# Performance work log

Hardware: AMD Instinct MI355X
Metric: run time of the kernel (lower is better)

## Reference

```python
import jax, jax.numpy as jnp
import numpy as np

NEG_SLOPE = 0.2   # PyG GATConv default leaky_relu slope
K_TOP = 50        # img_token_len
EPS = 1e-12


def _add_self_loops(ei, n):
    loop = jnp.arange(n, dtype=ei.dtype)
    return jnp.concatenate([ei, jnp.stack([loop, loop])], axis=1)


def _gcn(x, ei, W, b, n):
    ei = _add_self_loops(ei, n)
    src, dst = ei[0], ei[1]
    deg = jax.ops.segment_sum(jnp.ones_like(src, jnp.float32), dst, num_segments=n)
    dinv = jax.lax.rsqrt(jnp.maximum(deg, EPS))
    norm = dinv[src] * dinv[dst]                      # [E+N]
    h = x @ W                                         # [N, H]
    out = jax.ops.segment_sum(h[src] * norm[:, None], dst, num_segments=n)
    return out + b


def _gat(x, ei, W, b, a_src, a_dst, n):
    # PyG GATConv, heads=1, concat=True, with self loops; returns attention
    ei = _add_self_loops(ei, n)
    src, dst = ei[0], ei[1]
    h = x @ W                                         # [N, D]
    asrc = h @ a_src                                  # [N]
    adst = h @ a_dst                                  # [N]
    e = jax.nn.leaky_relu(asrc[src] + adst[dst], NEG_SLOPE)
    # segment softmax over incoming edges of each dst node
    m = jax.ops.segment_max(e, dst, num_segments=n)
    ex = jnp.exp(e - m[dst])
    s = jax.ops.segment_sum(ex, dst, num_segments=n)
    alpha = ex / s[dst]                               # [E+N]
    out = jax.ops.segment_sum(alpha[:, None] * h[src], dst, num_segments=n) + b
    return out, ei, alpha


def _patch_att(ei, alpha, n):
    # fused form of the original per-edge python loop: scatter-add alpha to
    # both endpoints, count contributions, divide (segment mean)
    src, dst = ei[0], ei[1]
    ones = jnp.ones_like(alpha)
    att = jax.ops.segment_sum(alpha, src, num_segments=n) + \
          jax.ops.segment_sum(alpha, dst, num_segments=n)
    cnt = jax.ops.segment_sum(ones, src, num_segments=n) + \
          jax.ops.segment_sum(ones, dst, num_segments=n)
    return att / cnt


def reference(x, edge_index, W_gcn, b_gcn, W_gat, b_gat, a_src, a_dst, W_proj, b_proj):
    B, N, _ = x.shape

    def per_graph(xi, ei):
        h = jax.nn.relu(_gcn(xi, ei, W_gcn, b_gcn, N))        # dropout: eval mode (identity)
        gnn_out, ei_sl, alpha = _gat(h, ei, W_gat, b_gat, a_src, a_dst, N)
        score = _patch_att(ei_sl, alpha, N)
        return gnn_out, score

    emb, scores = jax.vmap(per_graph)(x, edge_index)          # [B,N,256], [B,N]
    emb = emb @ W_proj + b_proj                               # img_proj -> [B,N,1024]
    emb = emb.reshape(-1, emb.shape[-1])                      # [B*N, 1024]
    scores = scores.reshape(-1)                               # [B*N]
    topk_scores, topk_idx = jax.lax.top_k(scores, K_TOP)
    topk_feats = emb[topk_idx]                                # [50, 1024]
    return topk_feats


def setup_inputs() -> dict:
    key = jax.random.key(0)
    ks = jax.random.split(key, 8)
    B, N, E, F, H, D, P = 256, 100, 1600, 2048, 512, 256, 1024
    return {
        "x": jax.random.normal(ks[0], (B, N, F), jnp.float32),
        "edge_index": jax.random.randint(ks[1], (B, 2, E), 0, N, dtype=jnp.int64),
        "W_gcn": jax.random.normal(ks[2], (F, H), jnp.float32) * (1.0 / np.sqrt(F)),
        "b_gcn": jnp.zeros((H,), jnp.float32),
        "W_gat": jax.random.normal(ks[3], (H, D), jnp.float32) * (1.0 / np.sqrt(H)),
        "b_gat": jnp.zeros((D,), jnp.float32),
        "a_src": jax.random.normal(ks[4], (D,), jnp.float32) * 0.1,
        "a_dst": jax.random.normal(ks[5], (D,), jnp.float32) * 0.1,
        "W_proj": jax.random.normal(ks[6], (D, P), jnp.float32) * (1.0 / np.sqrt(D)),
        "b_proj": jnp.zeros((P,), jnp.float32),
    }
```

## Files before the change

kernel.cpp:

```cpp
#include <hip/hip_runtime.h>
#include <hip/hip_bf16.h>
#include <stdint.h>

#define NB      256
#define NN      100
#define NE      1600
#define NEL     1700
#define FIN     2048
#define HG      512
#define DG      256
#define PO      1024
#define KTOP    50
#define NEG_SLOPE 0.2f

typedef __attribute__((ext_vector_type(8))) short bf16x8;
typedef __attribute__((ext_vector_type(4))) float f32x4;
typedef unsigned int u32;

__device__ inline ushort f2bf(float x) {
  unsigned u = __float_as_uint(x);
  return (ushort)((u + 0x7fffu + ((u >> 16) & 1u)) >> 16);
}
__device__ inline float bf2f(ushort b) {
  return __uint_as_float((unsigned)b << 16);
}

__device__ inline void gl16(const void* g, void* l) {
  __builtin_amdgcn_global_load_lds(
      (const __attribute__((address_space(1))) u32*)g,
      (__attribute__((address_space(3))) u32*)l, 16, 0, 0);
}

__device__ inline int swz(int row, int kc) {
  return row * 32 + ((((kc >> 3) ^ ((row >> 1) & 3)) << 3) | (kc & 7));
}

__global__ void tsplit_both(const float* __restrict__ Wg,
                            ushort* __restrict__ gh, ushort* __restrict__ gl_,
                            const float* __restrict__ Wa,
                            ushort* __restrict__ ah, ushort* __restrict__ al) {
  int e = blockIdx.x * 256 + threadIdx.x;
  if (e < HG * FIN) {
    int n = e >> 11, k = e & 2047;
    float v = Wg[(size_t)k * HG + n];
    ushort h = f2bf(v);
    gh[e] = h;
    gl_[e] = f2bf(v - bf2f(h));
  } else {
    int e2 = e - HG * FIN;
    if (e2 < DG * HG) {
      int n = e2 >> 9, k = e2 & 511;
      float v = Wa[(size_t)k * DG + n];
      ushort h = f2bf(v);
      ah[e2] = h;
      al[e2] = f2bf(v - bf2f(h));
    }
  }
}

template <int KSH>
__global__ __launch_bounds__(256, 2) void gemm_split_mfma(
    const float* __restrict__ A, const ushort* __restrict__ Bhi_t,
    const ushort* __restrict__ Blo_t, float* __restrict__ C, int M, int N) {
  constexpr int K = 1 << KSH;
  __shared__ ushort Ahi[128 * 32], Alo[128 * 32];
  __shared__ ushort Bsh[256 * 32], Bsl[256 * 32];
  const int tid = threadIdx.x;
  const int lane = tid & 63;
  const int wid = tid >> 6;
  const int wm0 = (wid & 1) * 64;
  const int wn0 = (wid >> 1) * 128;
  const int bm0 = blockIdx.y * 128, bn0 = blockIdx.x * 256;
  const int r16 = lane & 15, g16 = lane >> 4;
  f32x4 acc[4][8] = {};

  for (int k0 = 0; k0 < K; k0 += 32) {
    __syncthreads();
#pragma unroll
    for (int i = 0; i < 4; i++) {
      const int colb = wid * 64 + i * 16;
      const int col = colb + (lane >> 2);
      const int rot = (col >> 1) & 3;
      size_t go = (((size_t)(bn0 + col)) << KSH) + k0 + (((lane & 3) ^ rot) << 3);
      gl16(&Bhi_t[go], &Bsh[colb * 32]);
      gl16(&Blo_t[go], &Bsl[colb * 32]);
    }
#pragma unroll
    for (int u = 0; u < 4; u++) {
      int c = tid + u * 256;
      int row = c >> 3, kc = (c & 7) * 4;
      float4 v = *(const float4*)&A[(((size_t)(bm0 + row)) << KSH) + k0 + kc];
      ushort4 h, l;
      h.x = f2bf(v.x); l.x = f2bf(v.x - bf2f(h.x));
      h.y = f2bf(v.y); l.y = f2bf(v.y - bf2f(h.y));
      h.z = f2bf(v.z); l.z = f2bf(v.z - bf2f(h.z));
      h.w = f2bf(v.w); l.w = f2bf(v.w - bf2f(h.w));
      int o = swz(row, kc);
      *(ushort4*)&Ahi[o] = h;
      *(ushort4*)&Alo[o] = l;
    }
    __syncthreads();
    bf16x8 ahf[4], alf[4];
#pragma unroll
    for (int m = 0; m < 4; m++) {
      int o = swz(wm0 + m * 16 + r16, g16 * 8);
      ahf[m] = *(const bf16x8*)&Ahi[o];
      alf[m] = *(const bf16x8*)&Alo[o];
    }
#pragma unroll
    for (int n = 0; n < 8; n++) {
      int o = swz(wn0 + n * 16 + r16, g16 * 8);
      bf16x8 bh = *(const bf16x8*)&Bsh[o];
      bf16x8 bl = *(const bf16x8*)&Bsl[o];
#pragma unroll
      for (int m = 0; m < 4; m++) {
        acc[m][n] = __builtin_amdgcn_mfma_f32_16x16x32_bf16(ahf[m], bh, acc[m][n], 0, 0, 0);
        acc[m][n] = __builtin_amdgcn_mfma_f32_16x16x32_bf16(alf[m], bh, acc[m][n], 0, 0, 0);
        acc[m][n] = __builtin_amdgcn_mfma_f32_16x16x32_bf16(ahf[m], bl, acc[m][n], 0, 0, 0);
      }
    }
  }
  const int crow = g16 * 4;
#pragma unroll
  for (int m = 0; m < 4; m++)
#pragma unroll
    for (int n = 0; n < 8; n++)
#pragma unroll
      for (int r = 0; r < 4; r++)
        C[(size_t)(bm0 + wm0 + m * 16 + crow + r) * N + bn0 + wn0 + n * 16 + r16] =
            acc[m][n][r];
}

__global__ __launch_bounds__(256) void gcn_agg(
    const float* __restrict__ h0, const int* __restrict__ ei,
    const float* __restrict__ b_gcn, float* __restrict__ h1) {
  const int g = blockIdx.x, fc0 = blockIdx.y * 128, tid = threadIdx.x;
  __shared__ int   deg[NN];
  __shared__ float sdinv[NN];
  __shared__ int   offs[NN + 1], fill[NN];
  __shared__ int   eSrc[NEL];
  __shared__ float eNrm[NEL];
  const int* src = ei + (size_t)g * 2 * NE;
  const int* dst = src + NE;

  if (tid < NN) deg[tid] = 1;
  __syncthreads();
  for (int e = tid; e < NE; e += 256) atomicAdd(&deg[dst[e]], 1);
  __syncthreads();
  if (tid < NN) sdinv[tid] = rsqrtf(fmaxf((float)deg[tid], 1e-12f));
  if (tid == 0) {
    int s = 0;
    for (int n = 0; n < NN; n++) { offs[n] = s; s += deg[n]; }
    offs[NN] = s;
  }
  __syncthreads();
  if (tid < NN) fill[tid] = offs[tid];
  __syncthreads();
  for (int e = tid; e < NE; e += 256) {
    int s = src[e], d = dst[e];
    int p = atomicAdd(&fill[d], 1);
    eSrc[p] = s;
    eNrm[p] = sdinv[s] * sdinv[d];
  }
  if (tid < NN) {
    int p = atomicAdd(&fill[tid], 1);
    eSrc[p] = tid;
    eNrm[p] = sdinv[tid] * sdinv[tid];
  }
  __syncthreads();

  const float* h0g = h0 + (size_t)g * NN * HG + fc0;
  float* h1g = h1 + (size_t)g * NN * HG + fc0;
  const int grp = tid >> 5, tf = tid & 31;
  float4 bias = *(const float4*)&b_gcn[fc0 + tf * 4];
  for (int n = grp; n < NN; n += 8) {
    float4 acc = bias;
    const int p1 = offs[n + 1];
    for (int p = offs[n]; p < p1; p++) {
      float nr = eNrm[p];
      float4 hv = *(const float4*)&h0g[(size_t)eSrc[p] * HG + tf * 4];
      acc.x = fmaf(hv.x, nr, acc.x);
      acc.y = fmaf(hv.y, nr, acc.y);
      acc.z = fmaf(hv.z, nr, acc.z);
      acc.w = fmaf(hv.w, nr, acc.w);
    }
    acc.x = fmaxf(acc.x, 0.f); acc.y = fmaxf(acc.y, 0.f);
    acc.z = fmaxf(acc.z, 0.f); acc.w = fmaxf(acc.w, 0.f);
    *(float4*)&h1g[(size_t)n * HG + tf * 4] = acc;
  }
}

__device__ inline unsigned fmap(float f) {
  unsigned b = __float_as_uint(f);
  return (b & 0x80000000u) ? ~b : (b | 0x80000000u);
}
__device__ inline float funmap(unsigned u) {
  return __uint_as_float((u & 0x80000000u) ? (u & 0x7fffffffu) : ~u);
}

__global__ __launch_bounds__(256) void gat_alpha(
    const float* __restrict__ h2, const int* __restrict__ ei,
    const float* __restrict__ a_src, const float* __restrict__ a_dst,
    float* __restrict__ scores, int* __restrict__ csrO,
    int* __restrict__ csrS, float* __restrict__ csrA) {
  const int g = blockIdx.x, tid = threadIdx.x;
  __shared__ float    sAs[NN], sAd[NN];
  __shared__ unsigned mKey[NN];
  __shared__ float    sSum[NN], sAtt[NN];
  __shared__ int      sCnt[NN], degl[NN];
  __shared__ int      offs[NN + 1], fill[NN];
  __shared__ float    eV[NEL];
  __shared__ int      eS[NEL];
  __shared__ float    eA[NEL];
  const int* src = ei + (size_t)g * 2 * NE;
  const int* dst = src + NE;
  const float* h2g = h2 + (size_t)g * NN * DG;

  const int lane = tid & 63, wv = tid >> 6;
  for (int n = wv; n < NN; n += 4) {
    float4 hv  = *(const float4*)&h2g[(size_t)n * DG + lane * 4];
    float4 as4 = *(const float4*)&a_src[lane * 4];
    float4 ad4 = *(const float4*)&a_dst[lane * 4];
    float ps = hv.x * as4.x + hv.y * as4.y + hv.z * as4.z + hv.w * as4.w;
    float pd = hv.x * ad4.x + hv.y * ad4.y + hv.z * ad4.z + hv.w * ad4.w;
#pragma unroll
    for (int o = 32; o; o >>= 1) {
      ps += __shfl_down(ps, o);
      pd += __shfl_down(pd, o);
    }
    if (lane == 0) { sAs[n] = ps; sAd[n] = pd; }
  }
  if (tid < NN) {
    mKey[tid] = 0u; sSum[tid] = 0.f; sAtt[tid] = 0.f;
    sCnt[tid] = 0;  degl[tid] = 1;
  }
  __syncthreads();

  for (int i = tid; i < NEL; i += 256) {
    int s, d;
    if (i < NE) { s = src[i]; d = dst[i]; } else { s = d = i - NE; }
    float e = sAs[s] + sAd[d];
    e = (e > 0.f) ? e : NEG_SLOPE * e;
    eV[i] = e;
    atomicMax(&mKey[d], fmap(e));
    if (i < NE) atomicAdd(&degl[d], 1);
  }
  __syncthreads();

  for (int i = tid; i < NEL; i += 256) {
    int d = (i < NE) ? dst[i] : i - NE;
    float ex = expf(eV[i] - funmap(mKey[d]));
    eV[i] = ex;
    atomicAdd(&sSum[d], ex);
  }
  if (tid == 0) {
    int s = 0;
    for (int n = 0; n < NN; n++) { offs[n] = s; s += degl[n]; }
    offs[NN] = s;
  }
  __syncthreads();
  if (tid < NN) fill[tid] = offs[tid];
  __syncthreads();

  for (int i = tid; i < NEL; i += 256) {
    int s, d;
    if (i < NE) { s = src[i]; d = dst[i]; } else { s = d = i - NE; }
    float al = eV[i] / sSum[d];
    atomicAdd(&sAtt[s], al);
    atomicAdd(&sAtt[d], al);
    atomicAdd(&sCnt[s], 1);
    atomicAdd(&sCnt[d], 1);
    int p = atomicAdd(&fill[d], 1);
    eS[p] = s;
    eA[p] = al;
  }
  __syncthreads();

  if (tid < NN) scores[g * NN + tid] = sAtt[tid] / (float)sCnt[tid];
  if (tid <= NN) csrO[g * (NN + 1) + tid] = offs[tid];
  for (int i = tid; i < NEL; i += 256) {
    csrS[(size_t)g * NEL + i] = eS[i];
    csrA[(size_t)g * NEL + i] = eA[i];
  }
}

__global__ __launch_bounds__(256) void gat_agg(
    const float* __restrict__ h2, const int* __restrict__ csrO,
    const int* __restrict__ csrS, const float* __restrict__ csrA,
    const float* __restrict__ b_gat, float* __restrict__ out) {
  const int g = blockIdx.x, fc0 = blockIdx.y * 128, tid = threadIdx.x;
  __shared__ int   offs[NN + 1];
  __shared__ int   eS[NEL];
  __shared__ float eA[NEL];
  if (tid <= NN) offs[tid] = csrO[g * (NN + 1) + tid];
  for (int i = tid; i < NEL; i += 256) {
    eS[i] = csrS[(size_t)g * NEL + i];
    eA[i] = csrA[(size_t)g * NEL + i];
  }
  __syncthreads();

  const float* h2g = h2 + (size_t)g * NN * DG + fc0;
  float* outg = out + (size_t)g * NN * DG + fc0;
  const int grp = tid >> 5, tf = tid & 31;
  float4 bias = *(const float4*)&b_gat[fc0 + tf * 4];
  for (int n = grp; n < NN; n += 8) {
    float4 acc = bias;
    const int p1 = offs[n + 1];
    for (int p = offs[n]; p < p1; p++) {
      float al = eA[p];
      float4 hv = *(const float4*)&h2g[(size_t)eS[p] * DG + tf * 4];
      acc.x = fmaf(hv.x, al, acc.x);
      acc.y = fmaf(hv.y, al, acc.y);
      acc.z = fmaf(hv.z, al, acc.z);
      acc.w = fmaf(hv.w, al, acc.w);
    }
    *(float4*)&outg[(size_t)n * DG + tf * 4] = acc;
  }
}

__global__ __launch_bounds__(1024) void topk_radix(
    const float* __restrict__ scores, int* __restrict__ topk) {
  const int tid = threadIdx.x;
  unsigned key[25];
#pragma unroll
  for (int u = 0; u < 25; u++) key[u] = fmap(scores[tid + u * 1024]);

  __shared__ unsigned hist[16][256];
  __shared__ unsigned total[256], suff[257];
  __shared__ unsigned sPref;
  __shared__ int sNeed;
  const int wv = tid >> 6;
  unsigned pref = 0;
  int plen = 0, need = KTOP;
  for (int pass = 0; pass < 4; pass++) {
    const int shift = 24 - 8 * pass;
    for (int i = tid; i < 16 * 256; i += 1024) ((unsigned*)hist)[i] = 0;
    __syncthreads();
#pragma unroll
    for (int u = 0; u < 25; u++) {
      unsigned k = key[u];
      bool ok = (plen == 0) || ((k >> (32 - plen)) == (pref >> (32 - plen)));
      if (ok) atomicAdd(&hist[wv][(k >> shift) & 255], 1u);
    }
    __syncthreads();
    if (tid < 256) {
      unsigned s = 0;
#pragma unroll
      for (int w = 0; w < 16; w++) s += hist[w][tid];
      total[tid] = s;
      suff[tid] = s;
      if (tid == 0) suff[256] = 0;
    }
    __syncthreads();
    for (int st = 1; st < 256; st <<= 1) {
      unsigned v = 0;
      if (tid < 256) v = suff[tid] + ((tid + st < 256) ? suff[tid + st] : 0u);
      __syncthreads();
      if (tid < 256) suff[tid] = v;
      __syncthreads();
    }
    if (tid < 256) {
      unsigned s1 = suff[tid + 1];
      if (suff[tid] >= (unsigned)need && s1 < (unsigned)need) {
        sPref = pref | ((unsigned)tid << shift);
        sNeed = need - (int)s1;
      }
    }
    __syncthreads();
    pref = sPref;
    need = sNeed;
    plen += 8;
    __syncthreads();
  }

  const unsigned thr = pref;
  __shared__ int nGt;
  __shared__ unsigned long long cand[64];
  __shared__ int eqMin;
  if (tid == 0) nGt = 0;
  __syncthreads();
  unsigned eqmask = 0;
#pragma unroll
  for (int u = 0; u < 25; u++) {
    unsigned k = key[u];
    if (k > thr) {
      int p = atomicAdd(&nGt, 1);
      cand[p] = ((unsigned long long)k << 32) | (unsigned)(~(tid + u * 1024));
    } else if (k == thr) {
      eqmask |= 1u << u;
    }
  }
  __syncthreads();
  const int base = nGt;
  for (int r = 0; r < need; r++) {
    if (tid == 0) eqMin = 0x7fffffff;
    __syncthreads();
    int mymin = 0x7fffffff;
    unsigned mm = eqmask;
    while (mm) {
      int u = __ffs(mm) - 1;
      mm &= mm - 1;
      int idx = tid + u * 1024;
      if (idx < mymin) mymin = idx;
    }
#pragma unroll
    for (int o = 32; o; o >>= 1) {
      int ot = __shfl_down(mymin, o);
      if (ot < mymin) mymin = ot;
    }
    if ((tid & 63) == 0 && mymin != 0x7fffffff) atomicMin(&eqMin, mymin);
    __syncthreads();
    int sel = eqMin;
    if (tid == 0) topk[base + r] = sel;
    if ((sel & 1023) == tid) eqmask &= ~(1u << (sel >> 10));
    __syncthreads();
  }
  if (tid < 64) {
    unsigned long long c = (tid < base) ? cand[tid] : 0ull;
    for (int r = 0; r < base; r++) {
      unsigned long long m = c;
#pragma unroll
      for (int o = 32; o; o >>= 1) {
        unsigned long long t2 = __shfl_down(m, o);
        if (t2 > m) m = t2;
      }
      m = __shfl(m, 0);
      if (tid == 0) topk[r] = (int)(~(unsigned)m);
      if (c == m) c = 0ull;
    }
  }
}

__global__ __launch_bounds__(256) void proj_kernel(
    const float* __restrict__ gnn, const int* __restrict__ topk,
    const float* __restrict__ Wp, const float* __restrict__ bp,
    float* __restrict__ outp) {
  const int bi = blockIdx.x >> 2;
  const int c0 = (blockIdx.x & 3) * 256;
  const int tid = threadIdx.x;
  __shared__ float row[DG];
  const int node = topk[bi];
  row[tid] = gnn[(size_t)node * DG + tid];
  __syncthreads();
  float acc = 0.f;
#pragma unroll 8
  for (int k = 0; k < DG; k++)
    acc = fmaf(row[k], Wp[(size_t)k * PO + c0 + tid], acc);
  outp[(size_t)bi * PO + c0 + tid] = acc + bp[c0 + tid];
}

extern "C" void kernel_launch(void* const* d_in, const int* in_sizes, int n_in,
                              void* d_out, int out_size, void* d_ws,
                              size_t ws_size, hipStream_t stream) {
  const float* x      = (const float*)d_in[0];
  const int*   ei     = (const int*)d_in[1];
  const float* W_gcn  = (const float*)d_in[2];
  const float* b_gcn  = (const float*)d_in[3];
  const float* W_gat  = (const float*)d_in[4];
  const float* b_gat  = (const float*)d_in[5];
  const float* a_src  = (const float*)d_in[6];
  const float* a_dst  = (const float*)d_in[7];
  const float* W_proj = (const float*)d_in[8];
  const float* b_proj = (const float*)d_in[9];
  float* outp = (float*)d_out;

  char* ws = (char*)d_ws;
  float*  h0       = (float*)ws;
  float*  h2       = (float*)ws;
  float*  gnn      = (float*)(ws + 26214400);
  float*  h1       = (float*)(ws + 52428800);
  char*   wsc      = ws + 104857600;
  ushort* WgcnT_hi = (ushort*)(wsc);
  ushort* WgcnT_lo = (ushort*)(wsc + 2097152);
  ushort* WgatT_hi = (ushort*)(wsc + 4194304);
  ushort* WgatT_lo = (ushort*)(wsc + 4456448);
  float*  scores   = (float*)(wsc + 4718592);
  int*    topk     = (int*)(wsc + 4820992);
  int*    csrO     = (int*)(wsc + 4823040);
  int*    csrS     = (int*)(wsc + 4926464);
  float*  csrA     = (float*)(wsc + 6667264);

  const int M = NB * NN;

  tsplit_both<<<(HG * FIN + DG * HG + 255) / 256, 256, 0, stream>>>(
      W_gcn, WgcnT_hi, WgcnT_lo, W_gat, WgatT_hi, WgatT_lo);
  gemm_split_mfma<11><<<dim3(HG / 256, M / 128), 256, 0, stream>>>(
      x, WgcnT_hi, WgcnT_lo, h0, M, HG);
  gcn_agg<<<dim3(NB, 4), 256, 0, stream>>>(h0, ei, b_gcn, h1);
  gemm_split_mfma<9><<<dim3(DG / 256, M / 128), 256, 0, stream>>>(
      h1, WgatT_hi, WgatT_lo, h2, M, DG);
  gat_alpha<<<NB, 256, 0, stream>>>(h2, ei, a_src, a_dst, scores, csrO, csrS,
                                    csrA);
  gat_agg<<<dim3(NB, 2), 256, 0, stream>>>(h2, csrO, csrS, csrA, b_gat, gnn);
  topk_radix<<<1, 1024, 0, stream>>>(scores, topk);
  proj_kernel<<<KTOP * 4, 256, 0, stream>>>(gnn, topk, W_proj, b_proj, outp);
}
```

Before: 714.7 us.

## Replace sparse graph aggregation with dense per-graph adjacency MFMA matmuls

Builds a dense 100x100 normalized adjacency (GCN) or attention matrix (GAT) in LDS per graph and performs the aggregation as split-bf16 MFMA matmuls. GEMM epilogues now write feature-major outputs so the aggregation can load B tiles contiguously. The GAT alpha and aggregation kernels are fused, which removes the CSR build and its global round-trip. In exchange the kernels use heavy LDS, fewer blocks (one per graph), and do dense work on a sparse adjacency.

```diff
diff --git a/kernel.cpp b/kernel.cpp
--- a/kernel.cpp
+++ b/kernel.cpp
@@ -14,6 +14,7 @@
 #define NEG_SLOPE 0.2f
 
 typedef __attribute__((ext_vector_type(8))) short bf16x8;
+typedef __attribute__((ext_vector_type(8))) unsigned short u16x8;
 typedef __attribute__((ext_vector_type(4))) float f32x4;
 typedef unsigned int u32;
 
@@ -33,6 +34,16 @@
 
 __device__ inline int swz(int row, int kc) {
   return row * 32 + ((((kc >> 3) ^ ((row >> 1) & 3)) << 3) | (kc & 7));
+}
+
+__device__ inline void split8(float4 a, float4 b, u16x8& h, u16x8& l) {
+  float v[8] = {a.x, a.y, a.z, a.w, b.x, b.y, b.z, b.w};
+#pragma unroll
+  for (int i = 0; i < 8; i++) {
+    ushort hh = f2bf(v[i]);
+    h[i] = hh;
+    l[i] = f2bf(v[i] - bf2f(hh));
+  }
 }
 
 __global__ void tsplit_both(const float* __restrict__ Wg,
@@ -122,72 +133,123 @@
   }
   const int crow = g16 * 4;
 #pragma unroll
-  for (int m = 0; m < 4; m++)
-#pragma unroll
-    for (int n = 0; n < 8; n++)
-#pragma unroll
-      for (int r = 0; r < 4; r++)
-        C[(size_t)(bm0 + wm0 + m * 16 + crow + r) * N + bn0 + wn0 + n * 16 + r16] =
-            acc[m][n][r];
-}
-
-__global__ __launch_bounds__(256) void gcn_agg(
-    const float* __restrict__ h0, const int* __restrict__ ei,
+  for (int m = 0; m < 4; m++) {
+    int r0 = bm0 + wm0 + m * 16 + crow;
+    int gg = r0 / 100;
+    int nd = r0 - gg * 100;
+#pragma unroll
+    for (int n = 0; n < 8; n++) {
+      int col = bn0 + wn0 + n * 16 + r16;
+      if (nd <= 96) {
+        float4 v = {acc[m][n][0], acc[m][n][1], acc[m][n][2], acc[m][n][3]};
+        *(float4*)&C[((size_t)gg * N + col) * 100 + nd] = v;
+      } else {
+#pragma unroll
+        for (int q = 0; q < 4; q++) {
+          int nd2 = nd + q, g2 = gg;
+          if (nd2 >= 100) { nd2 -= 100; g2++; }
+          C[((size_t)g2 * N + col) * 100 + nd2] = acc[m][n][q];
+        }
+      }
+    }
+  }
+}
+
+template <int NF, bool RELU>
+__device__ __forceinline__ void agg_mfma_core(
+    const float* __restrict__ Bfm, const ushort* Sph, const ushort* Spl,
+    ushort* Bph, ushort* Bpl, const float* __restrict__ bias,
+    float* __restrict__ outg, int tid) {
+  const int lane = tid & 63, wid = tid >> 6;
+  const int r16 = lane & 15, g16 = lane >> 4;
+  for (int c = 0; c < NF / 64; c++) {
+    __syncthreads();
+    for (int t = tid; t < 1024; t += 256) {
+      int p = t >> 8, f = (t >> 2) & 63, ch = t & 3;
+      int k0 = p * 32 + ch * 8;
+      const float* rb = Bfm + (size_t)(c * 64 + f) * 100;
+      float4 v0 = {0.f, 0.f, 0.f, 0.f}, v1 = {0.f, 0.f, 0.f, 0.f};
+      if (k0 < 100) v0 = *(const float4*)&rb[k0];
+      if (k0 + 4 < 100) v1 = *(const float4*)&rb[k0 + 4];
+      u16x8 h, l;
+      split8(v0, v1, h, l);
+      int o = swz(f, ch * 8);
+      *(u16x8*)&Bph[p * 2048 + o] = h;
+      *(u16x8*)&Bpl[p * 2048 + o] = l;
+    }
+    __syncthreads();
+    f32x4 acc[7] = {};
+#pragma unroll
+    for (int ks = 0; ks < 4; ks++) {
+      int ob = ks * 2048 + swz(wid * 16 + r16, g16 * 8);
+      bf16x8 bh = *(const bf16x8*)&Bph[ob];
+      bf16x8 bl = *(const bf16x8*)&Bpl[ob];
+#pragma unroll
+      for (int mt = 0; mt < 7; mt++) {
+        int oa = ks * 3584 + swz(mt * 16 + r16, g16 * 8);
+        bf16x8 ah = *(const bf16x8*)&Sph[oa];
+        bf16x8 al = *(const bf16x8*)&Spl[oa];
+        acc[mt] = __builtin_amdgcn_mfma_f32_16x16x32_bf16(ah, bh, acc[mt], 0, 0, 0);
+        acc[mt] = __builtin_amdgcn_mfma_f32_16x16x32_bf16(al, bh, acc[mt], 0, 0, 0);
+        acc[mt] = __builtin_amdgcn_mfma_f32_16x16x32_bf16(ah, bl, acc[mt], 0, 0, 0);
+        acc[mt] = __builtin_amdgcn_mfma_f32_16x16x32_bf16(al, bl, acc[mt], 0, 0, 0);
+      }
+    }
+    const int col = c * 64 + wid * 16 + r16;
+    const float bv = bias[col];
+#pragma unroll
+    for (int mt = 0; mt < 7; mt++) {
+      int row0 = mt * 16 + g16 * 4;
+#pragma unroll
+      for (int q = 0; q < 4; q++) {
+        int row = row0 + q;
+        if (row < NN) {
+          float v = acc[mt][q] + bv;
+          if (RELU) v = fmaxf(v, 0.f);
+          outg[(size_t)row * NF + col] = v;
+        }
+      }
+    }
+  }
+}
+
+__global__ __launch_bounds__(256) void gcn_dense(
+    const float* __restrict__ h0fm, const int* __restrict__ ei,
     const float* __restrict__ b_gcn, float* __restrict__ h1) {
-  const int g = blockIdx.x, fc0 = blockIdx.y * 128, tid = threadIdx.x;
+  const int g = blockIdx.x, tid = threadIdx.x;
+  __shared__ __attribute__((aligned(16))) float  Sf32[14336];
+  __shared__ __attribute__((aligned(16))) ushort Sph[14336];
+  __shared__ __attribute__((aligned(16))) ushort Spl[14336];
+  __shared__ float dinv[NN];
   __shared__ int   deg[NN];
-  __shared__ float sdinv[NN];
-  __shared__ int   offs[NN + 1], fill[NN];
-  __shared__ int   eSrc[NEL];
-  __shared__ float eNrm[NEL];
+  ushort* Bph = (ushort*)Sf32;
+  ushort* Bpl = Bph + 8192;
   const int* src = ei + (size_t)g * 2 * NE;
   const int* dst = src + NE;
 
+  for (int i = tid; i < 14336; i += 256) Sf32[i] = 0.f;
   if (tid < NN) deg[tid] = 1;
   __syncthreads();
   for (int e = tid; e < NE; e += 256) atomicAdd(&deg[dst[e]], 1);
   __syncthreads();
-  if (tid < NN) sdinv[tid] = rsqrtf(fmaxf((float)deg[tid], 1e-12f));
-  if (tid == 0) {
-    int s = 0;
-    for (int n = 0; n < NN; n++) { offs[n] = s; s += deg[n]; }
-    offs[NN] = s;
-  }
-  __syncthreads();
-  if (tid < NN) fill[tid] = offs[tid];
+  if (tid < NN) dinv[tid] = rsqrtf((float)deg[tid]);
   __syncthreads();
   for (int e = tid; e < NE; e += 256) {
     int s = src[e], d = dst[e];
-    int p = atomicAdd(&fill[d], 1);
-    eSrc[p] = s;
-    eNrm[p] = sdinv[s] * sdinv[d];
-  }
-  if (tid < NN) {
-    int p = atomicAdd(&fill[tid], 1);
-    eSrc[p] = tid;
-    eNrm[p] = sdinv[tid] * sdinv[tid];
-  }
-  __syncthreads();
-
-  const float* h0g = h0 + (size_t)g * NN * HG + fc0;
-  float* h1g = h1 + (size_t)g * NN * HG + fc0;
-  const int grp = tid >> 5, tf = tid & 31;
-  float4 bias = *(const float4*)&b_gcn[fc0 + tf * 4];
-  for (int n = grp; n < NN; n += 8) {
-    float4 acc = bias;
-    const int p1 = offs[n + 1];
-    for (int p = offs[n]; p < p1; p++) {
-      float nr = eNrm[p];
-      float4 hv = *(const float4*)&h0g[(size_t)eSrc[p] * HG + tf * 4];
-      acc.x = fmaf(hv.x, nr, acc.x);
-      acc.y = fmaf(hv.y, nr, acc.y);
-      acc.z = fmaf(hv.z, nr, acc.z);
-      acc.w = fmaf(hv.w, nr, acc.w);
-    }
-    acc.x = fmaxf(acc.x, 0.f); acc.y = fmaxf(acc.y, 0.f);
-    acc.z = fmaxf(acc.z, 0.f); acc.w = fmaxf(acc.w, 0.f);
-    *(float4*)&h1g[(size_t)n * HG + tf * 4] = acc;
-  }
+    atomicAdd(&Sf32[d * 128 + s], dinv[s] * dinv[d]);
+  }
+  if (tid < NN) atomicAdd(&Sf32[tid * 128 + tid], dinv[tid] * dinv[tid]);
+  __syncthreads();
+  for (int i = tid; i < 14336; i += 256) {
+    int row = i >> 7, k = i & 127;
+    float v = Sf32[i];
+    ushort h = f2bf(v);
+    int o = (k >> 5) * 3584 + swz(row, k & 31);
+    Sph[o] = h;
+    Spl[o] = f2bf(v - bf2f(h));
+  }
+  agg_mfma_core<HG, true>(h0fm + (size_t)g * HG * 100, Sph, Spl, Bph, Bpl,
+                          b_gcn, h1 + (size_t)g * NN * HG, tid);
 }
 
 __device__ inline unsigned fmap(float f) {
@@ -198,41 +260,45 @@
   return __uint_as_float((u & 0x80000000u) ? (u & 0x7fffffffu) : ~u);
 }
 
-__global__ __launch_bounds__(256) void gat_alpha(
-    const float* __restrict__ h2, const int* __restrict__ ei,
+__global__ __launch_bounds__(256) void gat_fused(
+    const float* __restrict__ h2fm, const int* __restrict__ ei,
     const float* __restrict__ a_src, const float* __restrict__ a_dst,
-    float* __restrict__ scores, int* __restrict__ csrO,
-    int* __restrict__ csrS, float* __restrict__ csrA) {
+    const float* __restrict__ b_gat, float* __restrict__ gnn,
+    float* __restrict__ scores) {
   const int g = blockIdx.x, tid = threadIdx.x;
-  __shared__ float    sAs[NN], sAd[NN];
+  __shared__ __attribute__((aligned(16))) float  Sf32[14336];
+  __shared__ __attribute__((aligned(16))) ushort Sph[14336];
+  __shared__ __attribute__((aligned(16))) ushort Spl[14336];
+  __shared__ float    sAs[NN], sAd[NN], sSum[NN], sAtt[NN];
   __shared__ unsigned mKey[NN];
-  __shared__ float    sSum[NN], sAtt[NN];
-  __shared__ int      sCnt[NN], degl[NN];
-  __shared__ int      offs[NN + 1], fill[NN];
+  __shared__ int      sCnt[NN];
   __shared__ float    eV[NEL];
-  __shared__ int      eS[NEL];
-  __shared__ float    eA[NEL];
+  __shared__ float    part[512];
+  ushort* Bph = (ushort*)Sf32;
+  ushort* Bpl = Bph + 8192;
   const int* src = ei + (size_t)g * 2 * NE;
   const int* dst = src + NE;
-  const float* h2g = h2 + (size_t)g * NN * DG;
-
-  const int lane = tid & 63, wv = tid >> 6;
-  for (int n = wv; n < NN; n += 4) {
-    float4 hv  = *(const float4*)&h2g[(size_t)n * DG + lane * 4];
-    float4 as4 = *(const float4*)&a_src[lane * 4];
-    float4 ad4 = *(const float4*)&a_dst[lane * 4];
-    float ps = hv.x * as4.x + hv.y * as4.y + hv.z * as4.z + hv.w * as4.w;
-    float pd = hv.x * ad4.x + hv.y * ad4.y + hv.z * ad4.z + hv.w * ad4.w;
-#pragma unroll
-    for (int o = 32; o; o >>= 1) {
-      ps += __shfl_down(ps, o);
-      pd += __shfl_down(pd, o);
-    }
-    if (lane == 0) { sAs[n] = ps; sAd[n] = pd; }
-  }
+  const float* hb = h2fm + (size_t)g * DG * 100;
+
+  for (int i = tid; i < 14336; i += 256) Sf32[i] = 0.f;
+  if (tid < NN) { mKey[tid] = 0u; sSum[tid] = 0.f; sAtt[tid] = 0.f; sCnt[tid] = 0; }
+  {
+    int n = tid & 127, fg = tid >> 7;
+    float ps = 0.f, pd = 0.f;
+    if (n < NN) {
+      for (int f = fg * 128; f < fg * 128 + 128; f++) {
+        float hv = hb[(size_t)f * 100 + n];
+        ps = fmaf(hv, a_src[f], ps);
+        pd = fmaf(hv, a_dst[f], pd);
+      }
+    }
+    part[tid] = ps;
+    part[256 + tid] = pd;
+  }
+  __syncthreads();
   if (tid < NN) {
-    mKey[tid] = 0u; sSum[tid] = 0.f; sAtt[tid] = 0.f;
-    sCnt[tid] = 0;  degl[tid] = 1;
+    sAs[tid] = part[tid] + part[128 + tid];
+    sAd[tid] = part[256 + tid] + part[384 + tid];
   }
   __syncthreads();
 
@@ -243,25 +309,15 @@
     e = (e > 0.f) ? e : NEG_SLOPE * e;
     eV[i] = e;
     atomicMax(&mKey[d], fmap(e));
-    if (i < NE) atomicAdd(&degl[d], 1);
-  }
-  __syncthreads();
-
+  }
+  __syncthreads();
   for (int i = tid; i < NEL; i += 256) {
     int d = (i < NE) ? dst[i] : i - NE;
     float ex = expf(eV[i] - funmap(mKey[d]));
     eV[i] = ex;
     atomicAdd(&sSum[d], ex);
   }
-  if (tid == 0) {
-    int s = 0;
-    for (int n = 0; n < NN; n++) { offs[n] = s; s += degl[n]; }
-    offs[NN] = s;
-  }
-  __syncthreads();
-  if (tid < NN) fill[tid] = offs[tid];
-  __syncthreads();
-
+  __syncthreads();
   for (int i = tid; i < NEL; i += 256) {
     int s, d;
     if (i < NE) { s = src[i]; d = dst[i]; } else { s = d = i - NE; }
@@ -270,52 +326,20 @@
     atomicAdd(&sAtt[d], al);
     atomicAdd(&sCnt[s], 1);
     atomicAdd(&sCnt[d], 1);
-    int p = atomicAdd(&fill[d], 1);
-    eS[p] = s;
-    eA[p] = al;
-  }
-  __syncthreads();
-
+    atomicAdd(&Sf32[d * 128 + s], al);
+  }
+  __syncthreads();
   if (tid < NN) scores[g * NN + tid] = sAtt[tid] / (float)sCnt[tid];
-  if (tid <= NN) csrO[g * (NN + 1) + tid] = offs[tid];
-  for (int i = tid; i < NEL; i += 256) {
-    csrS[(size_t)g * NEL + i] = eS[i];
-    csrA[(size_t)g * NEL + i] = eA[i];
-  }
-}
-
-__global__ __launch_bounds__(256) void gat_agg(
-    const float* __restrict__ h2, const int* __restrict__ csrO,
-    const int* __restrict__ csrS, const float* __restrict__ csrA,
-    const float* __restrict__ b_gat, float* __restrict__ out) {
-  const int g = blockIdx.x, fc0 = blockIdx.y * 128, tid = threadIdx.x;
-  __shared__ int   offs[NN + 1];
-  __shared__ int   eS[NEL];
-  __shared__ float eA[NEL];
-  if (tid <= NN) offs[tid] = csrO[g * (NN + 1) + tid];
-  for (int i = tid; i < NEL; i += 256) {
-    eS[i] = csrS[(size_t)g * NEL + i];
-    eA[i] = csrA[(size_t)g * NEL + i];
-  }
-  __syncthreads();
-
-  const float* h2g = h2 + (size_t)g * NN * DG + fc0;
-  float* outg = out + (size_t)g * NN * DG + fc0;
-  const int grp = tid >> 5, tf = tid & 31;
-  float4 bias = *(const float4*)&b_gat[fc0 + tf * 4];
-  for (int n = grp; n < NN; n += 8) {
-    float4 acc = bias;
-    const int p1 = offs[n + 1];
-    for (int p = offs[n]; p < p1; p++) {
-      float al = eA[p];
-      float4 hv = *(const float4*)&h2g[(size_t)eS[p] * DG + tf * 4];
-      acc.x = fmaf(hv.x, al, acc.x);
-      acc.y = fmaf(hv.y, al, acc.y);
-      acc.z = fmaf(hv.z, al, acc.z);
-      acc.w = fmaf(hv.w, al, acc.w);
-    }
-    *(float4*)&outg[(size_t)n * DG + tf * 4] = acc;
-  }
+  for (int i = tid; i < 14336; i += 256) {
+    int row = i >> 7, k = i & 127;
+    float v = Sf32[i];
+    ushort h = f2bf(v);
+    int o = (k >> 5) * 3584 + swz(row, k & 31);
+    Sph[o] = h;
+    Spl[o] = f2bf(v - bf2f(h));
+  }
+  agg_mfma_core<DG, false>(hb, Sph, Spl, Bph, Bpl, b_gat,
+                           gnn + (size_t)g * NN * DG, tid);
 }
 
 __global__ __launch_bounds__(1024) void topk_radix(
@@ -465,8 +489,8 @@
   float* outp = (float*)d_out;
 
   char* ws = (char*)d_ws;
-  float*  h0       = (float*)ws;
-  float*  h2       = (float*)ws;
+  float*  h0fm     = (float*)ws;
+  float*  h2fm     = (float*)ws;
   float*  gnn      = (float*)(ws + 26214400);
   float*  h1       = (float*)(ws + 52428800);
   char*   wsc      = ws + 104857600;
@@ -476,22 +500,18 @@
   ushort* WgatT_lo = (ushort*)(wsc + 4456448);
   float*  scores   = (float*)(wsc + 4718592);
   int*    topk     = (int*)(wsc + 4820992);
-  int*    csrO     = (int*)(wsc + 4823040);
-  int*    csrS     = (int*)(wsc + 4926464);
-  float*  csrA     = (float*)(wsc + 6667264);
 
   const int M = NB * NN;
 
   tsplit_both<<<(HG * FIN + DG * HG + 255) / 256, 256, 0, stream>>>(
       W_gcn, WgcnT_hi, WgcnT_lo, W_gat, WgatT_hi, WgatT_lo);
   gemm_split_mfma<11><<<dim3(HG / 256, M / 128), 256, 0, stream>>>(
-      x, WgcnT_hi, WgcnT_lo, h0, M, HG);
-  gcn_agg<<<dim3(NB, 4), 256, 0, stream>>>(h0, ei, b_gcn, h1);
+      x, WgcnT_hi, WgcnT_lo, h0fm, M, HG);
+  gcn_dense<<<NB, 256, 0, stream>>>(h0fm, ei, b_gcn, h1);
   gemm_split_mfma<9><<<dim3(DG / 256, M / 128), 256, 0, stream>>>(
-      h1, WgatT_hi, WgatT_lo, h2, M, DG);
-  gat_alpha<<<NB, 256, 0, stream>>>(h2, ei, a_src, a_dst, scores, csrO, csrS,
-                                    csrA);
-  gat_agg<<<dim3(NB, 2), 256, 0, stream>>>(h2, csrO, csrS, csrA, b_gat, gnn);
+      h1, WgatT_hi, WgatT_lo, h2fm, M, DG);
+  gat_fused<<<NB, 256, 0, stream>>>(h2fm, ei, a_src, a_dst, b_gat, gnn,
+                                    scores);
   topk_radix<<<1, 1024, 0, stream>>>(scores, topk);
   proj_kernel<<<KTOP * 4, 256, 0, stream>>>(gnn, topk, W_proj, b_proj, outp);
 }
```

Result: faster. 648.5 us (-9.3%).
